# Kernel tuning notes

Hardware: AMD Instinct MI355X
Metric: run time of the kernel (lower is better)

Reference implementation:

```python
import jax, jax.numpy as jnp
import numpy as np

FP8_MAX = 448.0  # float8_e4m3fn max
NUM_HEADS = 16

def _fp8_quant_dequant(t):
    # per-(batch, head) symmetric scaling into fp8 e4m3 range, cast to fp8 and back
    amax = jnp.max(jnp.abs(t), axis=(-2, -1), keepdims=True)
    scale = FP8_MAX / jnp.maximum(amax, 1e-12)
    t8 = (t * scale).astype(jnp.float8_e4m3fn).astype(t.dtype)
    return t8 / scale

def setup_inputs() -> dict:
    key = jax.random.key(0)
    k1, k2, k3 = jax.random.split(key, 3)
    B, N, C = 2, 2048, 1024
    x = jax.random.normal(k1, (B, N, C), dtype=jnp.float32)
    w_qkv = jax.random.normal(k2, (C, 3 * C), dtype=jnp.float32) * (C ** -0.5)
    w_proj = jax.random.normal(k3, (C, C), dtype=jnp.float32) * (C ** -0.5)
    b_proj = jnp.zeros((C,), dtype=jnp.float32)
    return {"x": x, "w_qkv": w_qkv, "w_proj": w_proj, "b_proj": b_proj}

def reference(x, w_qkv, w_proj, b_proj):
    B, N, C = x.shape
    H = NUM_HEADS
    D = C // H
    scale = D ** -0.5
    qkv = (x @ w_qkv).reshape(B, N, 3, H, D).transpose(2, 0, 3, 1, 4)  # [3,B,H,N,D]
    q, k, v = qkv[0], qkv[1], qkv[2]
    # sage-style fp8 quantize/dequant of q and k fused into score computation
    q = _fp8_quant_dequant(q)
    k = _fp8_quant_dequant(k)
    scores = jnp.einsum('bhqd,bhkd->bhqk', q, k) * scale  # [B,H,N,N]
    causal = jnp.tril(jnp.ones((N, N), dtype=bool))
    scores = jnp.where(causal[None, None], scores, jnp.finfo(scores.dtype).min)
    attn = jax.nn.softmax(scores, axis=-1)
    out = jnp.einsum('bhqk,bhkd->bhqd', attn, v)  # [B,H,N,D]
    out = out.transpose(0, 2, 1, 3).reshape(B, N, C)
    return out @ w_proj + b_proj
```

## Files before the change

### kernel.cpp

```cpp
#include <hip/hip_runtime.h>

#define B_   2
#define N_   2048
#define C_   1024
#define H_   16
#define D_   64
#define BH_  (B_*H_)
#define NDH  (N_*D_)
#define M1   (B_*N_)

typedef __attribute__((ext_vector_type(4))) float    f32x4;
typedef __attribute__((ext_vector_type(8))) _Float16 f16x8;
typedef __attribute__((ext_vector_type(4))) _Float16 f16x4;
typedef __attribute__((ext_vector_type(2))) __fp16   fp16v2;

#define GLOAD_LDS(gp, lp) \
  __builtin_amdgcn_global_load_lds((const __attribute__((address_space(1))) void*)(gp), \
                                   (__attribute__((address_space(3))) void*)(lp), 16, 0, 0)

__global__ void k_cvt16(const float* __restrict__ in, _Float16* __restrict__ out, int n4) {
  int i = blockIdx.x * blockDim.x + threadIdx.x;
  if (i >= n4) return;
  float4 v = ((const float4*)in)[i];
  f16x4 o;
  o.x = (_Float16)v.x; o.y = (_Float16)v.y; o.z = (_Float16)v.z; o.w = (_Float16)v.w;
  ((f16x4*)out)[i] = o;
}

__global__ __launch_bounds__(256) void k_transmerge(const float* __restrict__ wq,
                                                    const float* __restrict__ wp,
                                                    _Float16* __restrict__ whT,
                                                    _Float16* __restrict__ wpT,
                                                    unsigned* __restrict__ amax_u) {
  if (blockIdx.x == 0 && threadIdx.x < 64) amax_u[threadIdx.x] = 0u;
  __shared__ _Float16 t[64][68];
  int idx = blockIdx.x;
  const float* in; _Float16* out; int Cc, cx, cy;
  if (idx < 768) { in = wq; out = whT; Cc = 3072; cx = idx % 48; cy = idx / 48; }
  else { idx -= 768; in = wp; out = wpT; Cc = 1024; cx = idx % 16; cy = idx / 16; }
  const int R = 1024;
  int c0 = cx * 64, r0 = cy * 64;
  int tid = threadIdx.x;
  int cq = tid & 15, rq = tid >> 4;
#pragma unroll
  for (int i = 0; i < 4; ++i) {
    int r = rq + i * 16;
    float4 v = *(const float4*)(in + (size_t)(r0 + r) * Cc + c0 + cq * 4);
    t[r][cq*4+0] = (_Float16)v.x;
    t[r][cq*4+1] = (_Float16)v.y;
    t[r][cq*4+2] = (_Float16)v.z;
    t[r][cq*4+3] = (_Float16)v.w;
  }
  __syncthreads();
#pragma unroll
  for (int i = 0; i < 4; ++i) {
    int c = rq + i * 16;
    f16x4 o;
    o.x = t[cq*4+0][c];
    o.y = t[cq*4+1][c];
    o.z = t[cq*4+2][c];
    o.w = t[cq*4+3][c];
    *(f16x4*)(out + (size_t)(c0 + c) * R + r0 + cq * 4) = o;
  }
}

__global__ __launch_bounds__(256) void k_gemm_qkv(const _Float16* __restrict__ A,
                                                  const _Float16* __restrict__ BT,
                                                  _Float16* __restrict__ qh,
                                                  _Float16* __restrict__ kh,
                                                  _Float16* __restrict__ vh,
                                                  unsigned* __restrict__ amax_u) {
  __shared__ __align__(16) _Float16 As[128 * 32];
  __shared__ __align__(16) _Float16 Bs[128 * 32];
  const int tid = threadIdx.x, lane = tid & 63, wave = tid >> 6;
  const int wm = wave >> 1, wn = wave & 1;
  const int mcol = lane & 15, quad = lane >> 4;
  const int m0 = blockIdx.x * 128, n0 = blockIdx.y * 128;
  f32x4 acc[4][4] = {};
  for (int k0 = 0; k0 < 1024; k0 += 32) {
#pragma unroll
    for (int r = 0; r < 2; ++r) {
      int c = tid + r * 256;
      int row = c >> 2, kc = c & 3;
      GLOAD_LDS(A  + (size_t)(m0 + row) * 1024 + k0 + kc * 8, &As[c * 8]);
      GLOAD_LDS(BT + (size_t)(n0 + row) * 1024 + k0 + kc * 8, &Bs[c * 8]);
    }
    __syncthreads();
    f16x8 af[4], bf[4];
#pragma unroll
    for (int tm = 0; tm < 4; ++tm)
      af[tm] = *(const f16x8*)&As[(wm * 64 + tm * 16 + mcol) * 32 + quad * 8];
#pragma unroll
    for (int tn = 0; tn < 4; ++tn)
      bf[tn] = *(const f16x8*)&Bs[(wn * 64 + tn * 16 + mcol) * 32 + quad * 8];
#pragma unroll
    for (int tm = 0; tm < 4; ++tm)
#pragma unroll
      for (int tn = 0; tn < 4; ++tn)
        acc[tm][tn] = __builtin_amdgcn_mfma_f32_16x16x32_f16(af[tm], bf[tn], acc[tm][tn], 0, 0, 0);
    __syncthreads();
  }
  const int sec = n0 >> 10;
  if (sec < 2) {
    _Float16* dst = sec ? kh : qh;
    float mxv = 0.f;
#pragma unroll
    for (int tm = 0; tm < 4; ++tm)
#pragma unroll
      for (int tn = 0; tn < 4; ++tn) {
        int rowb = m0 + wm * 64 + tm * 16 + quad * 4;
        int col = n0 + wn * 64 + tn * 16 + mcol;
        int cc = col & 1023, h = cc >> 6, d = cc & 63;
        int b = rowb >> 11, n = rowb & 2047;
        f32x4 a = acc[tm][tn];
        mxv = fmaxf(mxv, fmaxf(fmaxf(fabsf(a[0]), fabsf(a[1])),
                               fmaxf(fabsf(a[2]), fabsf(a[3]))));
        f16x4 o;
        o.x = (_Float16)a[0]; o.y = (_Float16)a[1];
        o.z = (_Float16)a[2]; o.w = (_Float16)a[3];
        *(f16x4*)&dst[(size_t)(b * 16 + h) * 131072 + (size_t)(n >> 5) * 2048 + d * 32 + (n & 31)] = o;
      }
#pragma unroll
    for (int off = 32; off; off >>= 1) mxv = fmaxf(mxv, __shfl_xor(mxv, off));
    if (lane == 0) {
      int head = ((n0 & 1023) >> 6) + wn;
      int plane = (m0 >> 11) * 16 + head;
      atomicMax(&amax_u[sec * 32 + plane], __float_as_uint(mxv));
    }
  } else {
#pragma unroll
    for (int tm = 0; tm < 4; ++tm)
#pragma unroll
      for (int tn = 0; tn < 4; ++tn) {
        int rowb = m0 + wm * 64 + tm * 16 + quad * 4;
        int col = n0 + wn * 64 + tn * 16 + mcol;
        int cc = col & 1023, h = cc >> 6, d = cc & 63;
        int b = rowb >> 11, n = rowb & 2047;
        f16x4 o;
        o.x = (_Float16)acc[tm][tn][0];
        o.y = (_Float16)acc[tm][tn][1];
        o.z = (_Float16)acc[tm][tn][2];
        o.w = (_Float16)acc[tm][tn][3];
        *(f16x4*)&vh[(size_t)(b * 16 + h) * 131072 + (size_t)(n >> 5) * 2048 + d * 32 + (n & 31)] = o;
      }
  }
}

__global__ __launch_bounds__(256) void k_quant(const _Float16* __restrict__ qh,
                                               const _Float16* __restrict__ kh,
                                               const float* __restrict__ amax,
                                               char* __restrict__ q8,
                                               char* __restrict__ k8) {
  __shared__ ushort T[32][72];
  int blk = blockIdx.x;
  int which = blk >> 11;
  int idx = blk & 2047;
  int bh = idx >> 6, chunk = idx & 63;
  const _Float16* src = (which ? kh : qh) + (size_t)bh * NDH + chunk * 2048;
  float s = 448.f / fmaxf(amax[which * 32 + bh], 1e-12f);
  int t = threadIdx.x;
  f16x8 v = *(const f16x8*)(src + t * 8);
  int d = t >> 2, kk0 = (t & 3) * 8;
#pragma unroll
  for (int j = 0; j < 8; ++j) T[kk0 + j][d] = ((const ushort*)&v)[j];
  __syncthreads();
  int r = t >> 3, d0 = (t & 7) * 8;
  f16x8 row = *(const f16x8*)&T[r][d0];
  float f[8];
#pragma unroll
  for (int j = 0; j < 8; ++j) f[j] = (float)((const _Float16*)&row)[j] * s;
  int lo = 0, hi = 0;
  lo = __builtin_amdgcn_cvt_pk_fp8_f32(f[0], f[1], lo, false);
  lo = __builtin_amdgcn_cvt_pk_fp8_f32(f[2], f[3], lo, true);
  hi = __builtin_amdgcn_cvt_pk_fp8_f32(f[4], f[5], hi, false);
  hi = __builtin_amdgcn_cvt_pk_fp8_f32(f[6], f[7], hi, true);
  int2 o; o.x = lo; o.y = hi;
  if (which == 0) {
    char* dst = q8 + (size_t)bh * NDH + (size_t)(chunk * 32 + r) * 64 + d0;
    *(int2*)dst = o;
  } else {
    int e = (r >> 2) & 1;
    int mc = (r >> 3) * 4 + (r & 3);
    int kb = d0 >> 5, dq = (d0 >> 3) & 3;
    char* dst = k8 + (size_t)bh * NDH + chunk * 2048 + (e * 2 + kb) * 512 + mc * 32 + dq * 8;
    *(int2*)dst = o;
  }
}

__global__ __launch_bounds__(256, 2) void k_flash(const char* __restrict__ q8,
                                                  const char* __restrict__ k8,
                                                  const _Float16* __restrict__ vh,
                                                  const float* __restrict__ amax,
                                                  _Float16* __restrict__ attn) {
  __shared__ float Osh[2][16][68];
  __shared__ float Msh[2][16], Lsh[2][16];
  const int bh = blockIdx.x;
  const int wave = threadIdx.x >> 6, lane = threadIdx.x & 63;
  const int mcol = lane & 15, quad = lane >> 4;
  const int pi = wave >> 1, role = wave & 1;
  const int pr = blockIdx.y * 2 + pi;
  const int ga = pr, gb = 127 - pr;
  const int ta = (ga >> 3) + 1;

  float sq = 448.f / fmaxf(amax[bh], 1e-12f);
  float sk = 448.f / fmaxf(amax[32 + bh], 1e-12f);
  const float c2 = (1.f / (sq * sk)) * 0.125f * 1.44269504089f;

  const size_t pbase = (size_t)bh * NDH;
  const char* kbase = k8 + pbase + mcol * 32 + quad * 8;
  const _Float16* vbase = vh + pbase + mcol * 32 + quad * 8;
  const int qrowA = ga * 16 + mcol, qrowB = gb * 16 + mcol;

  long aq0v, aq1v;
  { int qr = role ? qrowB : qrowA;
    const char* qp = q8 + pbase + (size_t)qr * 64;
    aq0v = *(const long*)(qp + quad * 8); aq1v = *(const long*)(qp + 32 + quad * 8); }

  f32x4 O[4] = {};
  float m_i = -3e38f, l_i = 0.f;
  const int b = bh >> 4, h = bh & 15;
  const int kq = quad * 8;
  const int NT = role ? 8 : 9;

  auto u_n0 = [&](int u) -> int {
    if (role) return (9 - ta + u) << 7;
    return (u < ta ? u : u - ta) << 7;
  };

  long kc[16], kn[16];
  {
    const char* kp = kbase + (size_t)(u_n0(0) >> 5) * 2048;
#pragma unroll
    for (int i = 0; i < 16; ++i) kc[i] = *(const long*)(kp + i * 512);
  }

  auto body = [&](int u, long (&cur)[16], long (&nxt)[16]) {
    const bool inA = (!role) && (u < ta);
    const int n0 = u_n0(u);
    const int qrow = inA ? qrowA : qrowB;
    const bool maskT = role ? (u == 7) : (u == ta - 1);
    const bool emitA = (!role) && (u == ta - 1);

    f32x4 s[4][2];
#pragma unroll
    for (int p = 0; p < 4; ++p)
#pragma unroll
      for (int e = 0; e < 2; ++e) {
        f32x4 z = {};
        z = __builtin_amdgcn_mfma_f32_16x16x32_fp8_fp8(cur[p * 4 + e * 2 + 0], aq0v, z, 0, 0, 0);
        z = __builtin_amdgcn_mfma_f32_16x16x32_fp8_fp8(cur[p * 4 + e * 2 + 1], aq1v, z, 0, 0, 0);
        s[p][e] = z;
      }
    f16x8 va[4][4];
    {
      const _Float16* vp = vbase + (size_t)(n0 >> 5) * 2048;
#pragma unroll
      for (int p = 0; p < 4; ++p)
#pragma unroll
        for (int dt = 0; dt < 4; ++dt)
          va[dt][p] = *(const f16x8*)(vp + p * 2048 + dt * 512);
    }
    if (u + 1 < NT) {
      const char* kp = kbase + (size_t)(u_n0(u + 1) >> 5) * 2048;
#pragma unroll
      for (int i = 0; i < 16; ++i) nxt[i] = *(const long*)(kp + i * 512);
    }
    if (maskT) {
#pragma unroll
      for (int p = 0; p < 4; ++p)
#pragma unroll
        for (int e = 0; e < 2; ++e)
#pragma unroll
          for (int r = 0; r < 4; ++r) {
            int key = n0 + p * 32 + kq + e * 4 + r;
            s[p][e][r] = (key <= qrow) ? s[p][e][r] : -3e38f;
          }
    }
    float fm[8];
#pragma unroll
    for (int p = 0; p < 4; ++p)
#pragma unroll
      for (int e = 0; e < 2; ++e) {
        f32x4 v = s[p][e];
        fm[p * 2 + e] = fmaxf(fmaxf(v[0], v[1]), fmaxf(v[2], v[3]));
      }
    float rm = fmaxf(fmaxf(fmaxf(fm[0], fm[1]), fmaxf(fm[2], fm[3])),
                     fmaxf(fmaxf(fm[4], fm[5]), fmaxf(fm[6], fm[7])));
    float mx = fmaxf(m_i, rm * c2);
    mx = fmaxf(mx, __shfl_xor(mx, 16));
    mx = fmaxf(mx, __shfl_xor(mx, 32));
    float alpha = exp2f(m_i - mx);
    m_i = mx;
    float fs[8];
    union { f16x8 v8; fp16v2 v2[4]; } pb[4];
#pragma unroll
    for (int p = 0; p < 4; ++p)
#pragma unroll
      for (int e = 0; e < 2; ++e) {
        float p0 = exp2f(__builtin_fmaf(s[p][e][0], c2, -mx));
        float p1 = exp2f(__builtin_fmaf(s[p][e][1], c2, -mx));
        float p2 = exp2f(__builtin_fmaf(s[p][e][2], c2, -mx));
        float p3 = exp2f(__builtin_fmaf(s[p][e][3], c2, -mx));
        pb[p].v2[e * 2 + 0] = __builtin_amdgcn_cvt_pkrtz(p0, p1);
        pb[p].v2[e * 2 + 1] = __builtin_amdgcn_cvt_pkrtz(p2, p3);
        fs[p * 2 + e] = (p0 + p1) + (p2 + p3);
      }
    float sum = ((fs[0] + fs[1]) + (fs[2] + fs[3])) + ((fs[4] + fs[5]) + (fs[6] + fs[7]));
    sum += __shfl_xor(sum, 16);
    sum += __shfl_xor(sum, 32);
    l_i = l_i * alpha + sum;
#pragma unroll
    for (int dt = 0; dt < 4; ++dt)
#pragma unroll
      for (int r = 0; r < 4; ++r)
        O[dt][r] *= alpha;
#pragma unroll
    for (int p = 0; p < 4; ++p)
#pragma unroll
      for (int dt = 0; dt < 4; ++dt)
        O[dt] = __builtin_amdgcn_mfma_f32_16x16x32_f16(va[dt][p], pb[p].v8, O[dt], 0, 0, 0);
    if (emitA) {
      float rl = 1.f / l_i;
      _Float16* op = attn + ((size_t)b * 2048 + qrowA) * 1024 + h * 64;
#pragma unroll
      for (int dt = 0; dt < 4; ++dt) {
        f16x4 o;
        o.x = (_Float16)(O[dt][0] * rl);
        o.y = (_Float16)(O[dt][1] * rl);
        o.z = (_Float16)(O[dt][2] * rl);
        o.w = (_Float16)(O[dt][3] * rl);
        *(f16x4*)(op + dt * 16 + quad * 4) = o;
        O[dt] = (f32x4){0.f, 0.f, 0.f, 0.f};
      }
      m_i = -3e38f; l_i = 0.f;
      const char* qp = q8 + pbase + (size_t)qrowB * 64;
      aq0v = *(const long*)(qp + quad * 8);
      aq1v = *(const long*)(qp + 32 + quad * 8);
    }
  };

#pragma unroll 1
  for (int u = 0; u < NT; u += 2) {
    body(u, kc, kn);
    if (u + 1 < NT) body(u + 1, kn, kc);
  }

  if (role) {
#pragma unroll
    for (int dt = 0; dt < 4; ++dt)
      *(f32x4*)&Osh[pi][mcol][dt * 16 + quad * 4] = O[dt];
    if (quad == 0) { Msh[pi][mcol] = m_i; Lsh[pi][mcol] = l_i; }
  }
  __syncthreads();
  if (!role) {
    float m1 = Msh[pi][mcol], l1 = Lsh[pi][mcol];
    float m = fmaxf(m_i, m1);
    float a0 = exp2f(m_i - m), a1 = exp2f(m1 - m);
    float rl = 1.f / (a0 * l_i + a1 * l1);
    _Float16* op = attn + ((size_t)b * 2048 + qrowB) * 1024 + h * 64;
#pragma unroll
    for (int dt = 0; dt < 4; ++dt) {
      f32x4 o1 = *(const f32x4*)&Osh[pi][mcol][dt * 16 + quad * 4];
      f16x4 o;
      o.x = (_Float16)((a0 * O[dt][0] + a1 * o1[0]) * rl);
      o.y = (_Float16)((a0 * O[dt][1] + a1 * o1[1]) * rl);
      o.z = (_Float16)((a0 * O[dt][2] + a1 * o1[2]) * rl);
      o.w = (_Float16)((a0 * O[dt][3] + a1 * o1[3]) * rl);
      *(f16x4*)(op + dt * 16 + quad * 4) = o;
    }
  }
}

__global__ __launch_bounds__(256) void k_gemm_out(const _Float16* __restrict__ A,
                                                  const _Float16* __restrict__ BT,
                                                  const float* __restrict__ bias,
                                                  float* __restrict__ out) {
  __shared__ __align__(16) _Float16 As[128 * 32];
  __shared__ __align__(16) _Float16 Bs[128 * 32];
  const int tid = threadIdx.x, lane = tid & 63, wave = tid >> 6;
  const int wm = wave >> 1, wn = wave & 1;
  const int mcol = lane & 15, quad = lane >> 4;
  const int m0 = blockIdx.x * 128, n0 = blockIdx.y * 128;
  f32x4 acc[4][4] = {};
  for (int k0 = 0; k0 < 1024; k0 += 32) {
#pragma unroll
    for (int r = 0; r < 2; ++r) {
      int c = tid + r * 256;
      int row = c >> 2, kc = c & 3;
      GLOAD_LDS(A  + (size_t)(m0 + row) * 1024 + k0 + kc * 8, &As[c * 8]);
      GLOAD_LDS(BT + (size_t)(n0 + row) * 1024 + k0 + kc * 8, &Bs[c * 8]);
    }
    __syncthreads();
    f16x8 af[4], bf[4];
#pragma unroll
    for (int tm = 0; tm < 4; ++tm)
      af[tm] = *(const f16x8*)&As[(wm * 64 + tm * 16 + mcol) * 32 + quad * 8];
#pragma unroll
    for (int tn = 0; tn < 4; ++tn)
      bf[tn] = *(const f16x8*)&Bs[(wn * 64 + tn * 16 + mcol) * 32 + quad * 8];
#pragma unroll
    for (int tm = 0; tm < 4; ++tm)
#pragma unroll
      for (int tn = 0; tn < 4; ++tn)
        acc[tm][tn] = __builtin_amdgcn_mfma_f32_16x16x32_f16(af[tm], bf[tn], acc[tm][tn], 0, 0, 0);
    __syncthreads();
  }
#pragma unroll
  for (int tm = 0; tm < 4; ++tm)
#pragma unroll
    for (int tn = 0; tn < 4; ++tn)
#pragma unroll
      for (int reg = 0; reg < 4; ++reg) {
        int row = m0 + wm * 64 + tm * 16 + quad * 4 + reg;
        int col = n0 + wn * 64 + tn * 16 + mcol;
        out[(size_t)row * 1024 + col] = acc[tm][tn][reg] + bias[col];
      }
}

extern "C" void kernel_launch(void* const* d_in, const int* in_sizes, int n_in,
                              void* d_out, int out_size, void* d_ws, size_t ws_size,
                              hipStream_t stream) {
  const float* x      = (const float*)d_in[0];
  const float* w_qkv  = (const float*)d_in[1];
  const float* w_proj = (const float*)d_in[2];
  const float* b_proj = (const float*)d_in[3];
  float* out = (float*)d_out;

  char* ws = (char*)d_ws;
  _Float16* xh   = (_Float16*)ws; ws += (size_t)M1 * C_ * 2;
  _Float16* whT  = (_Float16*)ws; ws += (size_t)3 * C_ * C_ * 2;
  _Float16* wpT  = (_Float16*)ws; ws += (size_t)C_ * C_ * 2;
  _Float16* qh   = (_Float16*)ws; ws += (size_t)BH_ * NDH * 2;
  _Float16* kh   = (_Float16*)ws; ws += (size_t)BH_ * NDH * 2;
  _Float16* vh   = (_Float16*)ws; ws += (size_t)BH_ * NDH * 2;
  char*     q8   = (char*)ws;     ws += (size_t)BH_ * NDH;
  char*     k8   = (char*)ws;     ws += (size_t)BH_ * NDH;
  _Float16* attn = (_Float16*)ws; ws += (size_t)M1 * C_ * 2;
  float*    amx  = (float*)ws;    ws += 256;

  k_cvt16<<<(M1 * C_ / 4 + 255) / 256, 256, 0, stream>>>(x, xh, M1 * C_ / 4);
  k_transmerge<<<1024, 256, 0, stream>>>(w_qkv, w_proj, whT, wpT, (unsigned*)amx);
  k_gemm_qkv<<<dim3(M1 / 128, 3 * C_ / 128), 256, 0, stream>>>(xh, whT, qh, kh, vh, (unsigned*)amx);
  k_quant<<<4096, 256, 0, stream>>>(qh, kh, amx, q8, k8);
  k_flash<<<dim3(32, 32), 256, 0, stream>>>(q8, k8, vh, amx, attn);
  k_gemm_out<<<dim3(M1 / 128, C_ / 128), 256, 0, stream>>>(attn, wpT, b_proj, out);
}
```

Before: 215.7 us.

## Software-pipeline QK score MFMAs one tile ahead of softmax and PV

Restructures the attention inner loop so the QK^T fp8 MFMAs for the next key tile are issued inside the current iteration, between the softmax exponentials and the PV MFMAs. Double-buffered score registers replace the double-buffered K registers, and both Q row fragments (A and B) are preloaded up front instead of being reloaded at the segment switch. The goal is to overlap matrix-core work with the exp/VALU softmax and to hide K load latency. The cost is higher VGPR pressure from holding two score tiles plus extra Q fragments, which could reduce occupancy or cause spills.

New measurement: 221.1 us. 2.5% more time.

```diff
diff --git a/kernel.cpp b/kernel.cpp
--- a/kernel.cpp
+++ b/kernel.cpp
@@ -211,10 +211,11 @@
   const _Float16* vbase = vh + pbase + mcol * 32 + quad * 8;
   const int qrowA = ga * 16 + mcol, qrowB = gb * 16 + mcol;
 
-  long aq0v, aq1v;
-  { int qr = role ? qrowB : qrowA;
-    const char* qp = q8 + pbase + (size_t)qr * 64;
-    aq0v = *(const long*)(qp + quad * 8); aq1v = *(const long*)(qp + 32 + quad * 8); }
+  long aqA0, aqA1, aqB0, aqB1;
+  { const char* qp = q8 + pbase + (size_t)qrowA * 64;
+    aqA0 = *(const long*)(qp + quad * 8); aqA1 = *(const long*)(qp + 32 + quad * 8); }
+  { const char* qp = q8 + pbase + (size_t)qrowB * 64;
+    aqB0 = *(const long*)(qp + quad * 8); aqB1 = *(const long*)(qp + 32 + quad * 8); }
 
   f32x4 O[4] = {};
   float m_i = -3e38f, l_i = 0.f;
@@ -226,31 +227,40 @@
     if (role) return (9 - ta + u) << 7;
     return (u < ta ? u : u - ta) << 7;
   };
-
-  long kc[16], kn[16];
+  auto in_b = [&](int u) -> bool { return role ? true : (u >= ta); };
+
+  long kc[16];
+  f32x4 s0[8], s1[8];
+
   {
     const char* kp = kbase + (size_t)(u_n0(0) >> 5) * 2048;
 #pragma unroll
     for (int i = 0; i < 16; ++i) kc[i] = *(const long*)(kp + i * 512);
-  }
-
-  auto body = [&](int u, long (&cur)[16], long (&nxt)[16]) {
-    const bool inA = (!role) && (u < ta);
+    const long a0 = in_b(0) ? aqB0 : aqA0, a1 = in_b(0) ? aqB1 : aqA1;
+#pragma unroll
+    for (int p = 0; p < 4; ++p)
+#pragma unroll
+      for (int e = 0; e < 2; ++e) {
+        f32x4 z = {};
+        z = __builtin_amdgcn_mfma_f32_16x16x32_fp8_fp8(kc[p * 4 + e * 2 + 0], a0, z, 0, 0, 0);
+        z = __builtin_amdgcn_mfma_f32_16x16x32_fp8_fp8(kc[p * 4 + e * 2 + 1], a1, z, 0, 0, 0);
+        s0[p * 2 + e] = z;
+      }
+  }
+
+  auto body = [&](int u, f32x4 (&scur)[8], f32x4 (&snxt)[8]) {
+    const bool haveN = (u + 1) < NT;
     const int n0 = u_n0(u);
-    const int qrow = inA ? qrowA : qrowB;
+    const bool inB = in_b(u);
+    const int qrow = inB ? qrowB : qrowA;
     const bool maskT = role ? (u == 7) : (u == ta - 1);
     const bool emitA = (!role) && (u == ta - 1);
 
-    f32x4 s[4][2];
-#pragma unroll
-    for (int p = 0; p < 4; ++p)
-#pragma unroll
-      for (int e = 0; e < 2; ++e) {
-        f32x4 z = {};
-        z = __builtin_amdgcn_mfma_f32_16x16x32_fp8_fp8(cur[p * 4 + e * 2 + 0], aq0v, z, 0, 0, 0);
-        z = __builtin_amdgcn_mfma_f32_16x16x32_fp8_fp8(cur[p * 4 + e * 2 + 1], aq1v, z, 0, 0, 0);
-        s[p][e] = z;
-      }
+    if (haveN) {
+      const char* kp = kbase + (size_t)(u_n0(u + 1) >> 5) * 2048;
+#pragma unroll
+      for (int i = 0; i < 16; ++i) kc[i] = *(const long*)(kp + i * 512);
+    }
     f16x8 va[4][4];
     {
       const _Float16* vp = vbase + (size_t)(n0 >> 5) * 2048;
@@ -260,11 +270,6 @@
         for (int dt = 0; dt < 4; ++dt)
           va[dt][p] = *(const f16x8*)(vp + p * 2048 + dt * 512);
     }
-    if (u + 1 < NT) {
-      const char* kp = kbase + (size_t)(u_n0(u + 1) >> 5) * 2048;
-#pragma unroll
-      for (int i = 0; i < 16; ++i) nxt[i] = *(const long*)(kp + i * 512);
-    }
     if (maskT) {
 #pragma unroll
       for (int p = 0; p < 4; ++p)
@@ -273,17 +278,15 @@
 #pragma unroll
           for (int r = 0; r < 4; ++r) {
             int key = n0 + p * 32 + kq + e * 4 + r;
-            s[p][e][r] = (key <= qrow) ? s[p][e][r] : -3e38f;
+            scur[p * 2 + e][r] = (key <= qrow) ? scur[p * 2 + e][r] : -3e38f;
           }
     }
     float fm[8];
 #pragma unroll
-    for (int p = 0; p < 4; ++p)
-#pragma unroll
-      for (int e = 0; e < 2; ++e) {
-        f32x4 v = s[p][e];
-        fm[p * 2 + e] = fmaxf(fmaxf(v[0], v[1]), fmaxf(v[2], v[3]));
-      }
+    for (int i = 0; i < 8; ++i) {
+      f32x4 v = scur[i];
+      fm[i] = fmaxf(fmaxf(v[0], v[1]), fmaxf(v[2], v[3]));
+    }
     float rm = fmaxf(fmaxf(fmaxf(fm[0], fm[1]), fmaxf(fm[2], fm[3])),
                      fmaxf(fmaxf(fm[4], fm[5]), fmaxf(fm[6], fm[7])));
     float mx = fmaxf(m_i, rm * c2);
@@ -297,28 +300,41 @@
     for (int p = 0; p < 4; ++p)
 #pragma unroll
       for (int e = 0; e < 2; ++e) {
-        float p0 = exp2f(__builtin_fmaf(s[p][e][0], c2, -mx));
-        float p1 = exp2f(__builtin_fmaf(s[p][e][1], c2, -mx));
-        float p2 = exp2f(__builtin_fmaf(s[p][e][2], c2, -mx));
-        float p3 = exp2f(__builtin_fmaf(s[p][e][3], c2, -mx));
+        float p0 = exp2f(__builtin_fmaf(scur[p * 2 + e][0], c2, -mx));
+        float p1 = exp2f(__builtin_fmaf(scur[p * 2 + e][1], c2, -mx));
+        float p2 = exp2f(__builtin_fmaf(scur[p * 2 + e][2], c2, -mx));
+        float p3 = exp2f(__builtin_fmaf(scur[p * 2 + e][3], c2, -mx));
         pb[p].v2[e * 2 + 0] = __builtin_amdgcn_cvt_pkrtz(p0, p1);
         pb[p].v2[e * 2 + 1] = __builtin_amdgcn_cvt_pkrtz(p2, p3);
         fs[p * 2 + e] = (p0 + p1) + (p2 + p3);
       }
+#pragma unroll
+    for (int dt = 0; dt < 4; ++dt)
+#pragma unroll
+      for (int r = 0; r < 4; ++r)
+        O[dt][r] *= alpha;
+    if (haveN) {
+      const bool inBn = in_b(u + 1);
+      const long a0 = inBn ? aqB0 : aqA0, a1 = inBn ? aqB1 : aqA1;
+#pragma unroll
+      for (int p = 0; p < 4; ++p)
+#pragma unroll
+        for (int e = 0; e < 2; ++e) {
+          f32x4 z = {};
+          z = __builtin_amdgcn_mfma_f32_16x16x32_fp8_fp8(kc[p * 4 + e * 2 + 0], a0, z, 0, 0, 0);
+          z = __builtin_amdgcn_mfma_f32_16x16x32_fp8_fp8(kc[p * 4 + e * 2 + 1], a1, z, 0, 0, 0);
+          snxt[p * 2 + e] = z;
+        }
+    }
+#pragma unroll
+    for (int p = 0; p < 4; ++p)
+#pragma unroll
+      for (int dt = 0; dt < 4; ++dt)
+        O[dt] = __builtin_amdgcn_mfma_f32_16x16x32_f16(va[dt][p], pb[p].v8, O[dt], 0, 0, 0);
     float sum = ((fs[0] + fs[1]) + (fs[2] + fs[3])) + ((fs[4] + fs[5]) + (fs[6] + fs[7]));
     sum += __shfl_xor(sum, 16);
     sum += __shfl_xor(sum, 32);
     l_i = l_i * alpha + sum;
-#pragma unroll
-    for (int dt = 0; dt < 4; ++dt)
-#pragma unroll
-      for (int r = 0; r < 4; ++r)
-        O[dt][r] *= alpha;
-#pragma unroll
-    for (int p = 0; p < 4; ++p)
-#pragma unroll
-      for (int dt = 0; dt < 4; ++dt)
-        O[dt] = __builtin_amdgcn_mfma_f32_16x16x32_f16(va[dt][p], pb[p].v8, O[dt], 0, 0, 0);
     if (emitA) {
       float rl = 1.f / l_i;
       _Float16* op = attn + ((size_t)b * 2048 + qrowA) * 1024 + h * 64;
@@ -333,16 +349,13 @@
         O[dt] = (f32x4){0.f, 0.f, 0.f, 0.f};
       }
       m_i = -3e38f; l_i = 0.f;
-      const char* qp = q8 + pbase + (size_t)qrowB * 64;
-      aq0v = *(const long*)(qp + quad * 8);
-      aq1v = *(const long*)(qp + 32 + quad * 8);
     }
   };
 
 #pragma unroll 1
   for (int u = 0; u < NT; u += 2) {
-    body(u, kc, kn);
-    if (u + 1 < NT) body(u + 1, kn, kc);
+    body(u, s0, s1);
+    if (u + 1 < NT) body(u + 1, s1, s0);
   }
 
   if (role) {
```

## Single-buffer K prefetch registers and raise flash kernel occupancy to three blocks

Applied to the files above, without the earlier changes.

The flash kernel drops the double-buffered K register arrays and instead reloads the single kc buffer right after the QK MFMAs consume it. This cuts register pressure so launch bounds can request three blocks per CU instead of two. The loop is no longer manually unrolled by two, and the row-sum reduction is moved after the PV MFMAs to overlap with them. The risk is less latency hiding for the K load within a wave, and possible spills under the tighter register budget.

After: 280.4 us. 30.0% more time.

```diff
diff --git a/kernel.cpp b/kernel.cpp
--- a/kernel.cpp
+++ b/kernel.cpp
@@ -187,7 +187,7 @@
   }
 }
 
-__global__ __launch_bounds__(256, 2) void k_flash(const char* __restrict__ q8,
+__global__ __launch_bounds__(256, 3) void k_flash(const char* __restrict__ q8,
                                                   const char* __restrict__ k8,
                                                   const _Float16* __restrict__ vh,
                                                   const float* __restrict__ amax,
@@ -227,30 +227,36 @@
     return (u < ta ? u : u - ta) << 7;
   };
 
-  long kc[16], kn[16];
+  long kc[16];
   {
     const char* kp = kbase + (size_t)(u_n0(0) >> 5) * 2048;
 #pragma unroll
     for (int i = 0; i < 16; ++i) kc[i] = *(const long*)(kp + i * 512);
   }
 
-  auto body = [&](int u, long (&cur)[16], long (&nxt)[16]) {
+  auto body = [&](int u) {
+    const bool haveN = (u + 1) < NT;
+    const int n0 = u_n0(u);
     const bool inA = (!role) && (u < ta);
-    const int n0 = u_n0(u);
     const int qrow = inA ? qrowA : qrowB;
     const bool maskT = role ? (u == 7) : (u == ta - 1);
     const bool emitA = (!role) && (u == ta - 1);
 
-    f32x4 s[4][2];
+    f32x4 s[8];
 #pragma unroll
     for (int p = 0; p < 4; ++p)
 #pragma unroll
       for (int e = 0; e < 2; ++e) {
         f32x4 z = {};
-        z = __builtin_amdgcn_mfma_f32_16x16x32_fp8_fp8(cur[p * 4 + e * 2 + 0], aq0v, z, 0, 0, 0);
-        z = __builtin_amdgcn_mfma_f32_16x16x32_fp8_fp8(cur[p * 4 + e * 2 + 1], aq1v, z, 0, 0, 0);
-        s[p][e] = z;
-      }
+        z = __builtin_amdgcn_mfma_f32_16x16x32_fp8_fp8(kc[p * 4 + e * 2 + 0], aq0v, z, 0, 0, 0);
+        z = __builtin_amdgcn_mfma_f32_16x16x32_fp8_fp8(kc[p * 4 + e * 2 + 1], aq1v, z, 0, 0, 0);
+        s[p * 2 + e] = z;
+      }
+    if (haveN) {
+      const char* kp = kbase + (size_t)(u_n0(u + 1) >> 5) * 2048;
+#pragma unroll
+      for (int i = 0; i < 16; ++i) kc[i] = *(const long*)(kp + i * 512);
+    }
     f16x8 va[4][4];
     {
       const _Float16* vp = vbase + (size_t)(n0 >> 5) * 2048;
@@ -260,11 +266,6 @@
         for (int dt = 0; dt < 4; ++dt)
           va[dt][p] = *(const f16x8*)(vp + p * 2048 + dt * 512);
     }
-    if (u + 1 < NT) {
-      const char* kp = kbase + (size_t)(u_n0(u + 1) >> 5) * 2048;
-#pragma unroll
-      for (int i = 0; i < 16; ++i) nxt[i] = *(const long*)(kp + i * 512);
-    }
     if (maskT) {
 #pragma unroll
       for (int p = 0; p < 4; ++p)
@@ -273,17 +274,15 @@
 #pragma unroll
           for (int r = 0; r < 4; ++r) {
             int key = n0 + p * 32 + kq + e * 4 + r;
-            s[p][e][r] = (key <= qrow) ? s[p][e][r] : -3e38f;
+            s[p * 2 + e][r] = (key <= qrow) ? s[p * 2 + e][r] : -3e38f;
           }
     }
     float fm[8];
 #pragma unroll
-    for (int p = 0; p < 4; ++p)
-#pragma unroll
-      for (int e = 0; e < 2; ++e) {
-        f32x4 v = s[p][e];
-        fm[p * 2 + e] = fmaxf(fmaxf(v[0], v[1]), fmaxf(v[2], v[3]));
-      }
+    for (int i = 0; i < 8; ++i) {
+      f32x4 v = s[i];
+      fm[i] = fmaxf(fmaxf(v[0], v[1]), fmaxf(v[2], v[3]));
+    }
     float rm = fmaxf(fmaxf(fmaxf(fm[0], fm[1]), fmaxf(fm[2], fm[3])),
                      fmaxf(fmaxf(fm[4], fm[5]), fmaxf(fm[6], fm[7])));
     float mx = fmaxf(m_i, rm * c2);
@@ -297,28 +296,28 @@
     for (int p = 0; p < 4; ++p)
 #pragma unroll
       for (int e = 0; e < 2; ++e) {
-        float p0 = exp2f(__builtin_fmaf(s[p][e][0], c2, -mx));
-        float p1 = exp2f(__builtin_fmaf(s[p][e][1], c2, -mx));
-        float p2 = exp2f(__builtin_fmaf(s[p][e][2], c2, -mx));
-        float p3 = exp2f(__builtin_fmaf(s[p][e][3], c2, -mx));
+        float p0 = exp2f(__builtin_fmaf(s[p * 2 + e][0], c2, -mx));
+        float p1 = exp2f(__builtin_fmaf(s[p * 2 + e][1], c2, -mx));
+        float p2 = exp2f(__builtin_fmaf(s[p * 2 + e][2], c2, -mx));
+        float p3 = exp2f(__builtin_fmaf(s[p * 2 + e][3], c2, -mx));
         pb[p].v2[e * 2 + 0] = __builtin_amdgcn_cvt_pkrtz(p0, p1);
         pb[p].v2[e * 2 + 1] = __builtin_amdgcn_cvt_pkrtz(p2, p3);
         fs[p * 2 + e] = (p0 + p1) + (p2 + p3);
       }
+#pragma unroll
+    for (int dt = 0; dt < 4; ++dt)
+#pragma unroll
+      for (int r = 0; r < 4; ++r)
+        O[dt][r] *= alpha;
+#pragma unroll
+    for (int p = 0; p < 4; ++p)
+#pragma unroll
+      for (int dt = 0; dt < 4; ++dt)
+        O[dt] = __builtin_amdgcn_mfma_f32_16x16x32_f16(va[dt][p], pb[p].v8, O[dt], 0, 0, 0);
     float sum = ((fs[0] + fs[1]) + (fs[2] + fs[3])) + ((fs[4] + fs[5]) + (fs[6] + fs[7]));
     sum += __shfl_xor(sum, 16);
     sum += __shfl_xor(sum, 32);
     l_i = l_i * alpha + sum;
-#pragma unroll
-    for (int dt = 0; dt < 4; ++dt)
-#pragma unroll
-      for (int r = 0; r < 4; ++r)
-        O[dt][r] *= alpha;
-#pragma unroll
-    for (int p = 0; p < 4; ++p)
-#pragma unroll
-      for (int dt = 0; dt < 4; ++dt)
-        O[dt] = __builtin_amdgcn_mfma_f32_16x16x32_f16(va[dt][p], pb[p].v8, O[dt], 0, 0, 0);
     if (emitA) {
       float rl = 1.f / l_i;
       _Float16* op = attn + ((size_t)b * 2048 + qrowA) * 1024 + h * 64;
@@ -340,10 +339,7 @@
   };
 
 #pragma unroll 1
-  for (int u = 0; u < NT; u += 2) {
-    body(u, kc, kn);
-    if (u + 1 < NT) body(u + 1, kn, kc);
-  }
+  for (int u = 0; u < NT; ++u) body(u);
 
   if (role) {
 #pragma unroll
```
